# Optimization experiments

Measured on AMD Instinct MI355X. Metric: run time of the kernel, lower is better.

The kernel has to match this reference:

```python
import jax, jax.numpy as jnp
import numpy as np

EPS = 1e-6
N_HEADS = 16
D_NOPE = 128   # qk_nope_head_dim == head_dim
D_ROPE = 64    # qk_rope_head_dim == head_dim // 2


def rmsnorm(x, g):
    # matches torch RMSNorm: normalize in fp32 then scale
    xf = x.astype(jnp.float32)
    n = xf * jax.lax.rsqrt(jnp.mean(xf * xf, axis=-1, keepdims=True) + EPS)
    return n.astype(x.dtype) * g


def rope(x):
    # x: [..., S, D]; rotary-embedding-torch convention: interleaved pairs, theta=10000
    S, D = x.shape[-2], x.shape[-1]
    freqs = 1.0 / (10000.0 ** (jnp.arange(0, D, 2, dtype=jnp.float32) / D))  # [D/2]
    ang = jnp.arange(S, dtype=jnp.float32)[:, None] * freqs                   # [S, D/2]
    ang = jnp.repeat(ang, 2, axis=-1)                                         # [S, D]
    cos, sin = jnp.cos(ang), jnp.sin(ang)
    x2 = x.reshape(*x.shape[:-1], D // 2, 2)
    xr = jnp.stack([-x2[..., 1], x2[..., 0]], axis=-1).reshape(x.shape)
    return x * cos + xr * sin


def setup_inputs() -> dict:
    key = jax.random.key(0)
    ks = jax.random.split(key, 9)
    def w(k, shape):
        return jax.random.normal(k, shape, dtype=jnp.float32) * (shape[0] ** -0.5)
    return {
        "x": jax.random.normal(ks[0], (2, 2048, 2048), dtype=jnp.float32),
        "w_dq": w(ks[1], (2048, 512)),
        "g_q": jnp.ones((512,), dtype=jnp.float32),
        "w_uq": w(ks[2], (512, 3072)),
        "w_dkv": w(ks[3], (2048, 512)),
        "g_kv": jnp.ones((512,), dtype=jnp.float32),
        "w_ukrope": w(ks[4], (2048, 64)),
        "w_uv": w(ks[5], (512, 2048)),
        "w_uknope": w(ks[6], (512, 2048)),
        "w_o": w(ks[7], (2048, 2048)),
    }


def reference(x, w_dq, g_q, w_uq, w_dkv, g_kv, w_ukrope, w_uv, w_uknope, w_o):
    B, S, _ = x.shape
    H, Dn, Dr = N_HEADS, D_NOPE, D_ROPE

    # low-rank KV path
    kv = rmsnorm(x @ w_dkv, g_kv)                                    # [B,S,512]
    k_nope = (kv @ w_uknope).reshape(B, S, H, Dn).transpose(0, 2, 1, 3)  # [B,H,S,Dn]
    v = (kv @ w_uv).reshape(B, S, H, Dn).transpose(0, 2, 1, 3)           # [B,H,S,Dn]
    k_rope = rope(x @ w_ukrope)                                      # [B,S,Dr] shared across heads

    # low-rank Q path
    q = rmsnorm(x @ w_dq, g_q) @ w_uq                                # [B,S,H*(Dn+Dr)]
    q = q.reshape(B, S, H, Dn + Dr).transpose(0, 2, 1, 3)            # [B,H,S,Dn+Dr]
    q_nope, q_rope = q[..., :Dn], rope(q[..., Dn:])

    # causal SDPA with head-shared rope keys folded into scores
    scale = 1.0 / jnp.sqrt(jnp.float32(Dn + Dr))
    scores = jnp.einsum("bhqd,bhkd->bhqk", q_nope, k_nope)
    scores = scores + jnp.einsum("bhqd,bkd->bhqk", q_rope, k_rope)
    scores = scores * scale
    causal = jnp.tril(jnp.ones((S, S), dtype=bool))
    scores = jnp.where(causal, scores, -jnp.inf)
    attn = jax.nn.softmax(scores, axis=-1)
    out = jnp.einsum("bhqk,bhkd->bhqd", attn, v)                     # [B,H,S,Dn]
    out = out.transpose(0, 2, 1, 3).reshape(B, S, H * Dn)
    return out @ w_o
```

## Files before the change

### kernel.cpp

```cpp
#include <hip/hip_runtime.h>
#include <hip/hip_bf16.h>


#define S_ 2048
#define H_ 16

typedef __bf16 bf16_t;
typedef __bf16 bf16x8 __attribute__((ext_vector_type(8)));
typedef __bf16 bf16x4_t __attribute__((ext_vector_type(4)));
typedef float f32x4 __attribute__((ext_vector_type(4)));

#define ASYNC_COPY16(gsrc, ldst)                                              \
  __builtin_amdgcn_global_load_lds(                                           \
      (const __attribute__((address_space(1))) void*)(gsrc),                  \
      (__attribute__((address_space(3))) void*)(ldst), 16, 0, 0)

#define QSCALE 0.1041177003f
#define FIXM 16.0f

struct TWDesc { const float* src; bf16_t* dst; int K, N, boff; };
struct TW7 { TWDesc d[7]; };

__global__ __launch_bounds__(256) void prep_all(const float* __restrict__ x,
                                                bf16_t* __restrict__ xb,
                                                float2* __restrict__ tab,
                                                TW7 t7) {
  __shared__ float t[32][33];
  int bid = blockIdx.x;
  int tid = threadIdx.x;
  if (bid < 8192) {
    int i = bid * 256 + tid;
    float4 v = ((const float4*)x)[i];
    bf16x4_t o = {(bf16_t)v.x, (bf16_t)v.y, (bf16_t)v.z, (bf16_t)v.w};
    ((bf16x4_t*)xb)[i] = o;
  } else if (bid < 8448) {
    int i = (bid - 8192) * 256 + tid;
    int j = i & 31, s = i >> 5;
    float freq = powf(10000.f, -(float)(2 * j) / 64.f);
    float ang = (float)s * freq;
    tab[i] = make_float2(cosf(ang), sinf(ang));
  } else {
    int e = 0;
#pragma unroll
    for (int i = 1; i < 7; i++)
      if (bid >= t7.d[i].boff) e = i;
    const float* src = t7.d[e].src;
    bf16_t* dst = t7.d[e].dst;
    int K = t7.d[e].K, N = t7.d[e].N;
    int lb = bid - t7.d[e].boff;
    int nx = N >> 5;
    int n0 = (lb % nx) * 32, k0 = (lb / nx) * 32;
    int tx = tid & 31, ty = tid >> 5;
#pragma unroll
    for (int i = 0; i < 4; i++)
      t[ty + i * 8][tx] = src[(size_t)(k0 + ty + i * 8) * N + n0 + tx];
    __syncthreads();
#pragma unroll
    for (int i = 0; i < 4; i++)
      dst[(size_t)(n0 + ty + i * 8) * K + k0 + tx] = (bf16_t)t[tx][ty + i * 8];
  }
}

template <typename OT, int MODE>
__global__ __launch_bounds__(256) void gemm_bt(const bf16_t* __restrict__ A,
                                               const bf16_t* __restrict__ Bt,
                                               OT* __restrict__ C, int M, int N,
                                               int K, int lda) {
  __shared__ bf16_t Asm[2][128 * 32];
  __shared__ bf16_t Bsm[2][128 * 32];
  int tid = threadIdx.x;
  int w = tid >> 6, lane = tid & 63;
  int lrow = lane & 15, lgrp = lane >> 4;
  int wr = w >> 1, wc = w & 1;
  int bm = blockIdx.y * 128, bn = blockIdx.x * 128;

  const bf16_t* Ab = A + (size_t)bm * lda;
  const bf16_t* Bb = Bt + (size_t)bn * K;

  int srow = (w << 5) + (lane >> 2);
  int schunk = lane & 3;

  int ra[4], rb[4];
#pragma unroll
  for (int m = 0; m < 4; m++) {
    int rowA = wr * 64 + m * 16 + lrow;
    ra[m] = rowA * 64 + ((lgrp * 16) ^ (((rowA >> 1) & 3) << 4));
    int rowB = wc * 64 + m * 16 + lrow;
    rb[m] = rowB * 64 + ((lgrp * 16) ^ (((rowB >> 1) & 3) << 4));
  }

  f32x4 acc[4][4] = {};

  auto stage = [&](int k0, int bufi) {
#pragma unroll
    for (int j = 0; j < 2; j++) {
      int row = srow + j * 16;
      int cs = schunk ^ ((row >> 1) & 3);
      ASYNC_COPY16(Ab + (size_t)row * lda + k0 + cs * 8,
                   (char*)Asm[bufi] + (w << 11) + (j << 10));
      ASYNC_COPY16(Bb + (size_t)row * K + k0 + cs * 8,
                   (char*)Bsm[bufi] + (w << 11) + (j << 10));
    }
  };

  const int niter = K >> 5;
  stage(0, 0);
  __syncthreads();
  int cur = 0;
#pragma unroll 1
  for (int kt = 0; kt < niter; kt++) {
    if (kt + 1 < niter) stage((kt + 1) << 5, cur ^ 1);
    bf16x8 af[4], bfr[4];
#pragma unroll
    for (int m = 0; m < 4; m++) {
      af[m] = *(const bf16x8*)((const char*)Asm[cur] + ra[m]);
      bfr[m] = *(const bf16x8*)((const char*)Bsm[cur] + rb[m]);
    }
#pragma unroll
    for (int m = 0; m < 4; m++)
#pragma unroll
      for (int n = 0; n < 4; n++)
        acc[m][n] =
            __builtin_amdgcn_mfma_f32_16x16x32_bf16(af[m], bfr[n], acc[m][n], 0, 0, 0);
    __syncthreads();
    cur ^= 1;
  }

#pragma unroll
  for (int m = 0; m < 4; m++)
#pragma unroll
    for (int n = 0; n < 4; n++)
#pragma unroll
      for (int j = 0; j < 4; j++) {
        int row = bm + wr * 64 + m * 16 + lgrp * 4 + j;
        int col = bn + wc * 64 + n * 16 + lrow;
        float val = acc[m][n][j];
        if (MODE == 0) {
          C[(size_t)row * N + col] = (OT)val;
        } else if (MODE == 6) {
          if (col < 1024) {
            ((bf16_t*)C)[(size_t)row * 1024 + col] = (bf16_t)val;
          } else if (col < 1088) {
            float* krf = (float*)((bf16_t*)C + (size_t)M * 1024);
            krf[(size_t)row * 64 + (col - 1024)] = val;
          }
        }
      }
}

__global__ __launch_bounds__(256) void gemm_qkv(const bf16_t* __restrict__ y,
                                                const bf16_t* __restrict__ uq_t,
                                                const bf16_t* __restrict__ ukn_t,
                                                bf16_t* __restrict__ Qp,
                                                bf16_t* __restrict__ Kp) {
  const int K = 512, lda = 1024;
  __shared__ bf16_t Asm[2][128 * 32];
  __shared__ bf16_t Bsm[2][128 * 32];
  int tid = threadIdx.x;
  int w = tid >> 6, lane = tid & 63;
  int lrow = lane & 15, lgrp = lane >> 4;
  int wr = w >> 1, wc = w & 1;
  int bnx = blockIdx.x;
  bool qpath = bnx < 24;
  const bf16_t* A = qpath ? y : (y + 512);
  const bf16_t* Bt = qpath ? uq_t : ukn_t;
  int bm = blockIdx.y * 128;
  int bn = (qpath ? bnx : bnx - 24) * 128;

  const bf16_t* Ab = A + (size_t)bm * lda;
  const bf16_t* Bb = Bt + (size_t)bn * K;

  int srow = (w << 5) + (lane >> 2);
  int schunk = lane & 3;

  int ra[4], rb[4];
#pragma unroll
  for (int m = 0; m < 4; m++) {
    int rowA = wr * 64 + m * 16 + lrow;
    ra[m] = rowA * 64 + ((lgrp * 16) ^ (((rowA >> 1) & 3) << 4));
    int rowB = wc * 64 + m * 16 + lrow;
    rb[m] = rowB * 64 + ((lgrp * 16) ^ (((rowB >> 1) & 3) << 4));
  }

  f32x4 acc[4][4] = {};

  auto stage = [&](int k0, int bufi) {
#pragma unroll
    for (int j = 0; j < 2; j++) {
      int row = srow + j * 16;
      int cs = schunk ^ ((row >> 1) & 3);
      ASYNC_COPY16(Ab + (size_t)row * lda + k0 + cs * 8,
                   (char*)Asm[bufi] + (w << 11) + (j << 10));
      ASYNC_COPY16(Bb + (size_t)row * K + k0 + cs * 8,
                   (char*)Bsm[bufi] + (w << 11) + (j << 10));
    }
  };

  const int niter = K >> 5;
  stage(0, 0);
  __syncthreads();
  int cur = 0;
#pragma unroll 1
  for (int kt = 0; kt < niter; kt++) {
    if (kt + 1 < niter) stage((kt + 1) << 5, cur ^ 1);
    bf16x8 af[4], bfr[4];
#pragma unroll
    for (int m = 0; m < 4; m++) {
      af[m] = *(const bf16x8*)((const char*)Asm[cur] + ra[m]);
      bfr[m] = *(const bf16x8*)((const char*)Bsm[cur] + rb[m]);
    }
#pragma unroll
    for (int m = 0; m < 4; m++)
#pragma unroll
      for (int n = 0; n < 4; n++)
        acc[m][n] =
            __builtin_amdgcn_mfma_f32_16x16x32_bf16(af[m], bfr[n], acc[m][n], 0, 0, 0);
    __syncthreads();
    cur ^= 1;
  }

#pragma unroll
  for (int m = 0; m < 4; m++)
#pragma unroll
    for (int n = 0; n < 4; n++) {
      int col = bn + wc * 64 + n * 16 + lrow;
      int row0 = bm + wr * 64 + m * 16 + lgrp * 4;
      if (!qpath && col >= 2048) {
        int c2 = col - 2048;
        int h = c2 >> 7, d = c2 & 127;
        bf16_t* VtP = Kp + (size_t)32 * S_ * 192;
        int b = row0 >> 11, s0 = row0 & (S_ - 1);
        bf16x4_t v4 = {(bf16_t)acc[m][n][0], (bf16_t)acc[m][n][1],
                       (bf16_t)acc[m][n][2], (bf16_t)acc[m][n][3]};
        *(bf16x4_t*)(VtP + ((size_t)((b << 4) + h) * 128 + d) * S_ + s0) = v4;
      } else {
#pragma unroll
        for (int j = 0; j < 4; j++) {
          int row = row0 + j;
          float val = acc[m][n][j];
          int b = row >> 11, s = row & (S_ - 1);
          if (qpath) {
            unsigned h = (unsigned)col / 192u, f = (unsigned)col % 192u;
            Qp[((size_t)((b << 4) + h) * S_ + s) * 192 + f] =
                (bf16_t)(val * QSCALE);
          } else {
            int h = col >> 7, d = col & 127;
            Kp[((size_t)((b << 4) + h) * S_ + s) * 192 + d] = (bf16_t)val;
          }
        }
      }
    }
}

__global__ __launch_bounds__(256) void rmsnorm_both(bf16_t* __restrict__ y,
                                                    const float* __restrict__ g_q,
                                                    const float* __restrict__ g_kv) {
  int bid = blockIdx.x;
  int row = bid >> 1, seg = bid & 1;
  const float* g = seg ? g_kv : g_q;
  bf16_t* p = y + (size_t)row * 1024 + seg * 512;
  int t = threadIdx.x;
  float v0 = (float)p[t], v1 = (float)p[t + 256];
  __shared__ float red[256];
  red[t] = v0 * v0 + v1 * v1;
  __syncthreads();
  for (int s = 128; s > 0; s >>= 1) {
    if (t < s) red[t] += red[t + s];
    __syncthreads();
  }
  float r = rsqrtf(red[0] / 512.f + 1e-6f);
  p[t] = (bf16_t)(v0 * r * g[t]);
  p[t + 256] = (bf16_t)(v1 * r * g[t + 256]);
}

__global__ __launch_bounds__(256) void rope_both(const float* __restrict__ krf,
                                                 const float2* __restrict__ tab,
                                                 bf16_t* __restrict__ Kp,
                                                 bf16_t* __restrict__ Qp) {
  int i = blockIdx.x * 256 + threadIdx.x;
  if (i < 4096 * 32) {
    int j = i & 31, row = i >> 5;
    int b = row >> 11, s = row & (S_ - 1);
    float v0 = krf[(size_t)row * 64 + 2 * j];
    float v1 = krf[(size_t)row * 64 + 2 * j + 1];
    float2 cs = tab[(s << 5) + j];
    bf16_t r0 = (bf16_t)(v0 * cs.x - v1 * cs.y);
    bf16_t r1 = (bf16_t)(v1 * cs.x + v0 * cs.y);
    union { bf16_t h[2]; unsigned u; } pk;
    pk.h[0] = r0; pk.h[1] = r1;
#pragma unroll
    for (int h = 0; h < 16; h++) {
      size_t base = ((size_t)((b << 4) + h) * S_ + s) * 192 + 128 + 2 * j;
      *(unsigned*)(Kp + base) = pk.u;
    }
  } else {
    int i2 = i - 4096 * 32;
    int j = i2 & 31;
    int s = (i2 >> 5) & (S_ - 1);
    int bh = i2 >> 16;
    float2 cs = tab[(s << 5) + j];
    size_t base = ((size_t)bh * S_ + s) * 192 + 128 + 2 * j;
    float x0 = (float)Qp[base], x1 = (float)Qp[base + 1];
    Qp[base] = (bf16_t)(x0 * cs.x - x1 * cs.y);
    Qp[base + 1] = (bf16_t)(x1 * cs.x + x0 * cs.y);
  }
}

__global__ __launch_bounds__(512) void flash_attn5(
    const bf16_t* __restrict__ Qp,
    const bf16_t* __restrict__ Kp,
    const bf16_t* __restrict__ Vt,
    bf16_t* __restrict__ o) {
  __shared__ alignas(16) char kls[2 * 64 * 384];
  __shared__ alignas(16) char vls[2 * 128 * 128];
  __shared__ alignas(16) bf16_t psh[8][16 * 64];

  int bid = blockIdx.x;
  int rest = bid >> 3;
  int p = rest & 7;
  int bh = (bid & 7) + ((rest >> 3) << 3);
  int b = bh >> 4;

  int tid = threadIdx.x;
  int w = tid >> 6;
  int lane = tid & 63;
  int lrow = lane & 15;
  int lgrp = lane >> 4;
  bf16_t* pw = &psh[w][0];

  const char* Kbh = (const char*)(Kp + (size_t)bh * S_ * 192);
  const char* Vbh = (const char*)(Vt + (size_t)bh * 128 * S_);

  int ksrc[3], vsrc[2];
#pragma unroll
  for (int r = 0; r < 3; r++) {
    int c = tid + r * 512;
    int row = c / 24, pos = c - row * 24;
    ksrc[r] = row * 384 + ((pos ^ (row & 7)) << 4);
  }
#pragma unroll
  for (int r = 0; r < 2; r++) {
    int c = tid + r * 512;
    int d = c >> 3, pos = c & 7;
    vsrc[r] = d * 4096 + ((pos ^ (d & 7)) << 4);
  }

  int kchk[6], vchk[2];
#pragma unroll
  for (int ks = 0; ks < 6; ks++)
    kchk[ks] = (((lgrp + ks * 4) ^ (lrow & 7)) << 4) + lrow * 384;
#pragma unroll
  for (int ks = 0; ks < 2; ks++)
    vchk[ks] = (((lgrp + ks * 4) ^ (lrow & 7)) << 4) + lrow * 128;

#pragma unroll 1
  for (int half = 0; half < 2; half++) {
    const int qt = half ? p : (15 - p);
    const int qb = qt * 128 + w * 16;
    const bf16_t* Qb = Qp + ((size_t)bh * S_ + qb) * 192;

    bf16x8 qf[6];
#pragma unroll
    for (int ks = 0; ks < 6; ks++)
      qf[ks] = *(const bf16x8*)(Qb + (size_t)lrow * 192 + ks * 32 + lgrp * 8);

    f32x4 acc[8];
#pragma unroll
    for (int i = 0; i < 8; i++) acc[i] = f32x4{0.f, 0.f, 0.f, 0.f};
    float lsum[4] = {0.f, 0.f, 0.f, 0.f};

    const int nk = 2 * qt + 2;
    {
      const char* kb = Kbh;
#pragma unroll
      for (int r = 0; r < 3; r++)
        ASYNC_COPY16(kb + ksrc[r], kls + (tid + r * 512) * 16);
#pragma unroll
      for (int r = 0; r < 2; r++)
        ASYNC_COPY16(Vbh + vsrc[r], vls + (tid + r * 512) * 16);
    }
    __syncthreads();

    int cur = 0;
#pragma unroll 1
    for (int kt = 0; kt < nk; kt++) {
      if (kt + 1 < nk) {
        const char* kb = Kbh + (size_t)(kt + 1) * (64 * 384);
        char* kd = kls + (cur ^ 1) * 24576;
#pragma unroll
        for (int r = 0; r < 3; r++)
          ASYNC_COPY16(kb + ksrc[r], kd + (tid + r * 512) * 16);
        const char* vb2 = Vbh + (size_t)(kt + 1) * 128;
        char* vd = vls + (cur ^ 1) * 16384;
#pragma unroll
        for (int r = 0; r < 2; r++)
          ASYNC_COPY16(vb2 + vsrc[r], vd + (tid + r * 512) * 16);
      }

      const char* kbuf = kls + cur * 24576;
      f32x4 sc[4];
#pragma unroll
      for (int cb = 0; cb < 4; cb++) {
        f32x4 s = f32x4{0.f, 0.f, 0.f, 0.f};
        const char* kp = kbuf + cb * 6144;
#pragma unroll
        for (int ks = 0; ks < 6; ks++) {
          bf16x8 kf = *(const bf16x8*)(kp + kchk[ks]);
          s = __builtin_amdgcn_mfma_f32_16x16x32_bf16(qf[ks], kf, s, 0, 0, 0);
        }
        sc[cb] = s;
      }
      if (kt >= 2 * qt) {
#pragma unroll
        for (int cb = 0; cb < 4; cb++)
#pragma unroll
          for (int r = 0; r < 4; r++) {
            int col = kt * 64 + cb * 16 + lrow;
            int row = qb + lgrp * 4 + r;
            if (col > row) sc[cb][r] = -1e30f;
          }
      }
#pragma unroll
      for (int r = 0; r < 4; r++) {
        float ps = 0.f;
#pragma unroll
        for (int cb = 0; cb < 4; cb++) {
          float e = exp2f(sc[cb][r] - FIXM);
          sc[cb][r] = e;
          ps += e;
        }
        lsum[r] += ps;
      }
#pragma unroll
      for (int r = 0; r < 4; r++) {
        int row = lgrp * 4 + r;
#pragma unroll
        for (int cb = 0; cb < 4; cb++) {
          int byte = (row * 128 + (cb * 16 + lrow) * 2) ^ ((row & 7) << 4);
          *(bf16_t*)((char*)pw + byte) = (bf16_t)sc[cb][r];
        }
      }
      bf16x8 pa[2];
#pragma unroll
      for (int ks = 0; ks < 2; ks++) {
        int byte = (lrow * 128 + ks * 64 + lgrp * 16) ^ ((lrow & 7) << 4);
        pa[ks] = *(const bf16x8*)((char*)pw + byte);
      }
      const char* vbuf = vls + cur * 16384;
#pragma unroll
      for (int cbv = 0; cbv < 8; cbv++) {
        const char* vp = vbuf + cbv * 2048;
        f32x4 a = acc[cbv];
#pragma unroll
        for (int ks = 0; ks < 2; ks++) {
          bf16x8 vf = *(const bf16x8*)(vp + vchk[ks]);
          a = __builtin_amdgcn_mfma_f32_16x16x32_bf16(pa[ks], vf, a, 0, 0, 0);
        }
        acc[cbv] = a;
      }
      __syncthreads();
      cur ^= 1;
    }
#pragma unroll
    for (int r = 0; r < 4; r++) {
      float s = lsum[r];
      s += __shfl_xor(s, 1);
      s += __shfl_xor(s, 2);
      s += __shfl_xor(s, 4);
      s += __shfl_xor(s, 8);
      float inv = 1.f / s;
      int row = qb + lgrp * 4 + r;
      bf16_t* op = o + (size_t)(b * S_ + row) * 2048 + (bh & 15) * 128;
#pragma unroll
      for (int cbv = 0; cbv < 8; cbv++)
        op[cbv * 16 + lrow] = (bf16_t)(acc[cbv][r] * inv);
    }
  }
}

extern "C" void kernel_launch(void* const* d_in, const int* in_sizes, int n_in,
                              void* d_out, int out_size, void* d_ws, size_t ws_size,
                              hipStream_t stream) {
  const float* x        = (const float*)d_in[0];
  const float* w_dq     = (const float*)d_in[1];
  const float* g_q      = (const float*)d_in[2];
  const float* w_uq     = (const float*)d_in[3];
  const float* w_dkv    = (const float*)d_in[4];
  const float* g_kv     = (const float*)d_in[5];
  const float* w_ukrope = (const float*)d_in[6];
  const float* w_uv     = (const float*)d_in[7];
  const float* w_uknope = (const float*)d_in[8];
  const float* w_o      = (const float*)d_in[9];
  float* out = (float*)d_out;

  const int M = 4096;
  bf16_t* wb = (bf16_t*)d_ws;
  size_t off = 0;
  bf16_t* xb   = wb + off; off += (size_t)M * 2048;
  bf16_t* y    = wb + off; off += (size_t)M * 1024;
  float*  krf  = (float*)(wb + off); off += (size_t)M * 128;
  bf16_t* dq_t = wb + off; off += (size_t)512 * 2048;
  bf16_t* dkv_t= wb + off; off += (size_t)512 * 2048;
  bf16_t* ukr_t= wb + off; off += (size_t)128 * 2048;
  bf16_t* uq_t = wb + off; off += (size_t)3072 * 512;
  bf16_t* ukn_t= wb + off; off += (size_t)2048 * 512;
  bf16_t* uv_t = wb + off; off += (size_t)2048 * 512;
  bf16_t* o_t  = wb + off; off += (size_t)2048 * 2048;
  bf16_t* Qp   = wb + off; off += (size_t)32 * S_ * 192;
  bf16_t* Kp   = wb + off; off += (size_t)32 * S_ * 192;
  bf16_t* Vt   = wb + off; off += (size_t)32 * 128 * S_;
  float2* tab  = (float2*)(wb + off); off += (size_t)S_ * 32 * 4;
  bf16_t* ao = xb;
  (void)dkv_t; (void)ukr_t; (void)uv_t;

  dim3 blk(256);
  TW7 t7;
  t7.d[0] = {w_dq,     dq_t,  2048, 512,  8448};
  t7.d[1] = {w_dkv,    dkv_t, 2048, 512,  9472};
  t7.d[2] = {w_ukrope, ukr_t, 2048, 64,   10496};
  t7.d[3] = {w_uq,     uq_t,  512,  3072, 10624};
  t7.d[4] = {w_uknope, ukn_t, 512,  2048, 12160};
  t7.d[5] = {w_uv,     uv_t,  512,  2048, 13184};
  t7.d[6] = {w_o,      o_t,   2048, 2048, 14208};
  prep_all<<<18304, blk, 0, stream>>>(x, xb, tab, t7);
  gemm_bt<bf16_t, 6><<<dim3(9, 32), blk, 0, stream>>>(xb, dq_t, y, M, 1152, 2048,
                                                      2048);
  rmsnorm_both<<<8192, blk, 0, stream>>>(y, g_q, g_kv);
  gemm_qkv<<<dim3(56, 32), blk, 0, stream>>>(y, uq_t, ukn_t, Qp, Kp);
  rope_both<<<8704, blk, 0, stream>>>(krf, tab, Kp, Qp);
  flash_attn5<<<256, dim3(512), 0, stream>>>(Qp, Kp, Vt, ao);
  gemm_bt<float, 0><<<dim3(16, 32), blk, 0, stream>>>(ao, o_t, out, M, 2048, 2048,
                                                      2048);
}
```

Before: 254.0 us.

## Switch flash attention to 32x32x16 MFMA tiles with four waves per block

The attention kernel moves from 16x16x32 MFMA with 8 waves of 16 query rows each to 32x32x16 MFMA with 4 waves of 32 query rows each. The K/V tile loads, the P staging layout in shared memory and the output indexing are reworked to match. The goal is fewer LDS fragment reads per FLOP and better MFMA throughput. The constant-max subtraction before exp2 is also dropped. The cost is half as many resident waves per CU, so less latency hiding, plus more register pressure and some overflow risk in the unnormalised exponentials.

New measurement: 286.2 us. 12.7% more time.

```diff
diff --git a/kernel.cpp b/kernel.cpp
--- a/kernel.cpp
+++ b/kernel.cpp
@@ -9,6 +9,7 @@
 typedef __bf16 bf16x8 __attribute__((ext_vector_type(8)));
 typedef __bf16 bf16x4_t __attribute__((ext_vector_type(4)));
 typedef float f32x4 __attribute__((ext_vector_type(4)));
+typedef float f32x16 __attribute__((ext_vector_type(16)));
 
 #define ASYNC_COPY16(gsrc, ldst)                                              \
   __builtin_amdgcn_global_load_lds(                                           \
@@ -16,7 +17,6 @@
       (__attribute__((address_space(3))) void*)(ldst), 16, 0, 0)
 
 #define QSCALE 0.1041177003f
-#define FIXM 16.0f
 
 struct TWDesc { const float* src; bf16_t* dst; int K, N, boff; };
 struct TW7 { TWDesc d[7]; };
@@ -306,14 +306,14 @@
   }
 }
 
-__global__ __launch_bounds__(512) void flash_attn5(
+__global__ __launch_bounds__(256) void flash_attn6(
     const bf16_t* __restrict__ Qp,
     const bf16_t* __restrict__ Kp,
     const bf16_t* __restrict__ Vt,
     bf16_t* __restrict__ o) {
   __shared__ alignas(16) char kls[2 * 64 * 384];
   __shared__ alignas(16) char vls[2 * 128 * 128];
-  __shared__ alignas(16) bf16_t psh[8][16 * 64];
+  __shared__ alignas(16) bf16_t psh[4][32 * 64];
 
   int bid = blockIdx.x;
   int rest = bid >> 3;
@@ -324,60 +324,59 @@
   int tid = threadIdx.x;
   int w = tid >> 6;
   int lane = tid & 63;
-  int lrow = lane & 15;
-  int lgrp = lane >> 4;
+  int l31 = lane & 31;
+  int hi = lane >> 5;
   bf16_t* pw = &psh[w][0];
 
   const char* Kbh = (const char*)(Kp + (size_t)bh * S_ * 192);
   const char* Vbh = (const char*)(Vt + (size_t)bh * 128 * S_);
 
-  int ksrc[3], vsrc[2];
-#pragma unroll
-  for (int r = 0; r < 3; r++) {
-    int c = tid + r * 512;
+  int ksrc[6], vsrc[4];
+#pragma unroll
+  for (int r = 0; r < 6; r++) {
+    int c = tid + r * 256;
     int row = c / 24, pos = c - row * 24;
     ksrc[r] = row * 384 + ((pos ^ (row & 7)) << 4);
   }
 #pragma unroll
-  for (int r = 0; r < 2; r++) {
-    int c = tid + r * 512;
+  for (int r = 0; r < 4; r++) {
+    int c = tid + r * 256;
     int d = c >> 3, pos = c & 7;
     vsrc[r] = d * 4096 + ((pos ^ (d & 7)) << 4);
   }
 
-  int kchk[6], vchk[2];
-#pragma unroll
-  for (int ks = 0; ks < 6; ks++)
-    kchk[ks] = (((lgrp + ks * 4) ^ (lrow & 7)) << 4) + lrow * 384;
-#pragma unroll
-  for (int ks = 0; ks < 2; ks++)
-    vchk[ks] = (((lgrp + ks * 4) ^ (lrow & 7)) << 4) + lrow * 128;
+  int krowoff[2];
+#pragma unroll
+  for (int cb = 0; cb < 2; cb++) krowoff[cb] = (cb * 32 + l31) * 384;
+  int kxor = l31 & 7;
 
 #pragma unroll 1
   for (int half = 0; half < 2; half++) {
     const int qt = half ? p : (15 - p);
-    const int qb = qt * 128 + w * 16;
+    const int qb = qt * 128 + w * 32;
     const bf16_t* Qb = Qp + ((size_t)bh * S_ + qb) * 192;
 
-    bf16x8 qf[6];
-#pragma unroll
-    for (int ks = 0; ks < 6; ks++)
-      qf[ks] = *(const bf16x8*)(Qb + (size_t)lrow * 192 + ks * 32 + lgrp * 8);
-
-    f32x4 acc[8];
-#pragma unroll
-    for (int i = 0; i < 8; i++) acc[i] = f32x4{0.f, 0.f, 0.f, 0.f};
-    float lsum[4] = {0.f, 0.f, 0.f, 0.f};
+    bf16x8 qf[12];
+#pragma unroll
+    for (int ks = 0; ks < 12; ks++)
+      qf[ks] = *(const bf16x8*)(Qb + (size_t)l31 * 192 + ks * 16 + hi * 8);
+
+    f32x16 acc[4];
+#pragma unroll
+    for (int i = 0; i < 4; i++) acc[i] = (f32x16)(0.f);
+    float lsum[16];
+#pragma unroll
+    for (int i = 0; i < 16; i++) lsum[i] = 0.f;
 
     const int nk = 2 * qt + 2;
     {
       const char* kb = Kbh;
 #pragma unroll
-      for (int r = 0; r < 3; r++)
-        ASYNC_COPY16(kb + ksrc[r], kls + (tid + r * 512) * 16);
-#pragma unroll
-      for (int r = 0; r < 2; r++)
-        ASYNC_COPY16(Vbh + vsrc[r], vls + (tid + r * 512) * 16);
+      for (int r = 0; r < 6; r++)
+        ASYNC_COPY16(kb + ksrc[r], kls + (tid + r * 256) * 16);
+#pragma unroll
+      for (int r = 0; r < 4; r++)
+        ASYNC_COPY16(Vbh + vsrc[r], vls + (tid + r * 256) * 16);
     }
     __syncthreads();
 
@@ -388,92 +387,96 @@
         const char* kb = Kbh + (size_t)(kt + 1) * (64 * 384);
         char* kd = kls + (cur ^ 1) * 24576;
 #pragma unroll
-        for (int r = 0; r < 3; r++)
-          ASYNC_COPY16(kb + ksrc[r], kd + (tid + r * 512) * 16);
+        for (int r = 0; r < 6; r++)
+          ASYNC_COPY16(kb + ksrc[r], kd + (tid + r * 256) * 16);
         const char* vb2 = Vbh + (size_t)(kt + 1) * 128;
         char* vd = vls + (cur ^ 1) * 16384;
 #pragma unroll
-        for (int r = 0; r < 2; r++)
-          ASYNC_COPY16(vb2 + vsrc[r], vd + (tid + r * 512) * 16);
+        for (int r = 0; r < 4; r++)
+          ASYNC_COPY16(vb2 + vsrc[r], vd + (tid + r * 256) * 16);
       }
 
       const char* kbuf = kls + cur * 24576;
-      f32x4 sc[4];
-#pragma unroll
-      for (int cb = 0; cb < 4; cb++) {
-        f32x4 s = f32x4{0.f, 0.f, 0.f, 0.f};
-        const char* kp = kbuf + cb * 6144;
-#pragma unroll
-        for (int ks = 0; ks < 6; ks++) {
-          bf16x8 kf = *(const bf16x8*)(kp + kchk[ks]);
-          s = __builtin_amdgcn_mfma_f32_16x16x32_bf16(qf[ks], kf, s, 0, 0, 0);
+      f32x16 sc[2];
+#pragma unroll
+      for (int cb = 0; cb < 2; cb++) {
+        f32x16 s = (f32x16)(0.f);
+        const char* kp = kbuf + krowoff[cb];
+#pragma unroll
+        for (int ks = 0; ks < 12; ks++) {
+          int chunk = (ks * 2 + hi) ^ kxor;
+          bf16x8 kf = *(const bf16x8*)(kp + (chunk << 4));
+          s = __builtin_amdgcn_mfma_f32_32x32x16_bf16(qf[ks], kf, s, 0, 0, 0);
         }
         sc[cb] = s;
       }
       if (kt >= 2 * qt) {
 #pragma unroll
-        for (int cb = 0; cb < 4; cb++)
-#pragma unroll
-          for (int r = 0; r < 4; r++) {
-            int col = kt * 64 + cb * 16 + lrow;
-            int row = qb + lgrp * 4 + r;
-            if (col > row) sc[cb][r] = -1e30f;
+        for (int cb = 0; cb < 2; cb++)
+#pragma unroll
+          for (int reg = 0; reg < 16; reg++) {
+            int col = kt * 64 + cb * 32 + l31;
+            int row = qb + (reg & 3) + 8 * (reg >> 2) + 4 * hi;
+            if (col > row) sc[cb][reg] = -1e30f;
           }
       }
 #pragma unroll
-      for (int r = 0; r < 4; r++) {
-        float ps = 0.f;
-#pragma unroll
-        for (int cb = 0; cb < 4; cb++) {
-          float e = exp2f(sc[cb][r] - FIXM);
-          sc[cb][r] = e;
-          ps += e;
+      for (int reg = 0; reg < 16; reg++) {
+        float e0 = exp2f(sc[0][reg]);
+        float e1 = exp2f(sc[1][reg]);
+        sc[0][reg] = e0;
+        sc[1][reg] = e1;
+        lsum[reg] += e0 + e1;
+      }
+#pragma unroll
+      for (int cb = 0; cb < 2; cb++) {
+        int pcol = cb * 32 + l31;
+        int csw = ((pcol >> 3) ^ 0) << 4;
+        (void)csw;
+#pragma unroll
+        for (int reg = 0; reg < 16; reg++) {
+          int prow = (reg & 3) + 8 * (reg >> 2) + 4 * hi;
+          int byte = prow * 128 + (((pcol >> 3) ^ (prow & 7)) << 4) + (pcol & 7) * 2;
+          *(bf16_t*)((char*)pw + byte) = (bf16_t)sc[cb][reg];
         }
-        lsum[r] += ps;
-      }
-#pragma unroll
-      for (int r = 0; r < 4; r++) {
-        int row = lgrp * 4 + r;
-#pragma unroll
-        for (int cb = 0; cb < 4; cb++) {
-          int byte = (row * 128 + (cb * 16 + lrow) * 2) ^ ((row & 7) << 4);
-          *(bf16_t*)((char*)pw + byte) = (bf16_t)sc[cb][r];
+      }
+      bf16x8 pa[4];
+#pragma unroll
+      for (int ks = 0; ks < 4; ks++) {
+        int chunk = (ks * 2 + hi) ^ (l31 & 7);
+        pa[ks] = *(const bf16x8*)((char*)pw + l31 * 128 + (chunk << 4));
+      }
+      const char* vbuf = vls + cur * 16384;
+#pragma unroll
+      for (int db = 0; db < 4; db++) {
+        int vr = db * 32 + l31;
+        const char* vp = vbuf + vr * 128;
+        f32x16 a = acc[db];
+#pragma unroll
+        for (int ks = 0; ks < 4; ks++) {
+          int chunk = (ks * 2 + hi) ^ (vr & 7);
+          bf16x8 vf = *(const bf16x8*)(vp + (chunk << 4));
+          a = __builtin_amdgcn_mfma_f32_32x32x16_bf16(pa[ks], vf, a, 0, 0, 0);
         }
-      }
-      bf16x8 pa[2];
-#pragma unroll
-      for (int ks = 0; ks < 2; ks++) {
-        int byte = (lrow * 128 + ks * 64 + lgrp * 16) ^ ((lrow & 7) << 4);
-        pa[ks] = *(const bf16x8*)((char*)pw + byte);
-      }
-      const char* vbuf = vls + cur * 16384;
-#pragma unroll
-      for (int cbv = 0; cbv < 8; cbv++) {
-        const char* vp = vbuf + cbv * 2048;
-        f32x4 a = acc[cbv];
-#pragma unroll
-        for (int ks = 0; ks < 2; ks++) {
-          bf16x8 vf = *(const bf16x8*)(vp + vchk[ks]);
-          a = __builtin_amdgcn_mfma_f32_16x16x32_bf16(pa[ks], vf, a, 0, 0, 0);
-        }
-        acc[cbv] = a;
+        acc[db] = a;
       }
       __syncthreads();
       cur ^= 1;
     }
 #pragma unroll
-    for (int r = 0; r < 4; r++) {
-      float s = lsum[r];
+    for (int reg = 0; reg < 16; reg++) {
+      float s = lsum[reg];
       s += __shfl_xor(s, 1);
       s += __shfl_xor(s, 2);
       s += __shfl_xor(s, 4);
       s += __shfl_xor(s, 8);
+      s += __shfl_xor(s, 16);
       float inv = 1.f / s;
-      int row = qb + lgrp * 4 + r;
+      int row = qb + (reg & 3) + 8 * (reg >> 2) + 4 * hi;
       bf16_t* op = o + (size_t)(b * S_ + row) * 2048 + (bh & 15) * 128;
 #pragma unroll
-      for (int cbv = 0; cbv < 8; cbv++)
-        op[cbv * 16 + lrow] = (bf16_t)(acc[cbv][r] * inv);
+      for (int db = 0; db < 4; db++)
+        op[db * 32 + l31] = (bf16_t)(acc[db][reg] * inv);
     }
   }
 }
@@ -528,7 +531,7 @@
   rmsnorm_both<<<8192, blk, 0, stream>>>(y, g_q, g_kv);
   gemm_qkv<<<dim3(56, 32), blk, 0, stream>>>(y, uq_t, ukn_t, Qp, Kp);
   rope_both<<<8704, blk, 0, stream>>>(krf, tab, Kp, Qp);
-  flash_attn5<<<256, dim3(512), 0, stream>>>(Qp, Kp, Vt, ao);
+  flash_attn6<<<256, blk, 0, stream>>>(Qp, Kp, Vt, ao);
   gemm_bt<float, 0><<<dim3(16, 32), blk, 0, stream>>>(ao, o_t, out, M, 2048, 2048,
                                                       2048);
 }
```
